# Optimization experiments

Hardware: AMD Instinct MI355X
Metric: run time of the kernel (lower is better)

Reference implementation:

```python
import jax, jax.numpy as jnp
import numpy as np

T = 4096; D = 768; V = 32000; L = 4; EPS = 1e-5


def _ln(x, g, b):
    m = jnp.mean(x, axis=-1, keepdims=True)
    v = jnp.mean((x - m) ** 2, axis=-1, keepdims=True)
    return (x - m) * jax.lax.rsqrt(v + EPS) * g + b


def _qgelu(x):
    return x * jax.nn.sigmoid(1.702 * x)


def setup_inputs() -> dict:
    key = jax.random.key(0)
    ks = jax.random.split(key, 10)
    s = 0.02
    return {
        "idx": jax.random.randint(ks[0], (T,), 0, V),
        "wte": jax.random.normal(ks[1], (V, D)) * s,
        "rb_ln_g": jnp.ones((D,)), "rb_ln_b": jnp.zeros((D,)),
        "rb_fc_w": jax.random.normal(ks[2], (D, 4 * D)) * s,
        "rb_fc_b": jnp.zeros((4 * D,)),
        "rb_proj_w": jax.random.normal(ks[3], (4 * D, D)) * s,
        "rb_proj_b": jnp.zeros((D,)),
        "lnf_g": jnp.ones((D,)), "lnf_b": jnp.zeros((D,)),
        "lm_head_w": jax.random.normal(ks[4], (D, V)) * s,
        "mb_ln_g": jnp.ones((L, 2 * D)), "mb_ln_b": jnp.zeros((L, 2 * D)),
        "mb_fc_w": jax.random.normal(ks[5], (L, 2 * D, 4 * D)) * s,
        "mb_fc_b": jnp.zeros((L, 4 * D)),
        "mb_proj_w": jax.random.normal(ks[6], (L, 4 * D, D)) * s,
        "mb_proj_b": jnp.zeros((L, D)),
        "op_w": jax.random.normal(ks[7], (L, D, D)) * s,
        "op_b": jnp.zeros((L, D)),
        "lns_g": jnp.ones((L, D)), "lns_b": jnp.zeros((L, D)),
        "heads_w": jax.random.normal(ks[8], (L, D, V)) * s,
    }


def reference(idx, wte, rb_ln_g, rb_ln_b, rb_fc_w, rb_fc_b, rb_proj_w, rb_proj_b,
              lnf_g, lnf_b, lm_head_w, mb_ln_g, mb_ln_b, mb_fc_w, mb_fc_b,
              mb_proj_w, mb_proj_b, op_w, op_b, lns_g, lns_b, heads_w):
    # token embedding (dropout is identity in eval) + initial residual block
    x = wte[idx]  # [T, D]
    h = _ln(x, rb_ln_g, rb_ln_b)
    x = x + _qgelu(h @ rb_fc_w + rb_fc_b) @ rb_proj_w + rb_proj_b
    x = _ln(x, lnf_g, lnf_b)
    logits = x @ lm_head_w  # [T, V]

    # targets=None path: pred_targets = cat(idx[1:], [-1])
    pred_targets = jnp.concatenate([idx[1:], jnp.full((1,), -1, idx.dtype)])
    pos = jnp.arange(T)
    skey = jax.random.key(42)

    for i in range(L):  # static small loop over layers
        j = i + 1
        # multinomial(softmax(logits), 1) == categorical(logits)
        idx_next = jax.random.categorical(jax.random.fold_in(skey, i), logits)
        # positions p where the sample matched the next-token target and p < T - j
        mask = (idx_next == pred_targets) & (pos < T - j)  # [T] bool
        # x2[p] = x[p + j] (padded); compute merge densely, select with mask
        x2 = jnp.concatenate([x[j:], jnp.zeros((j, D), x.dtype)], axis=0)
        h = _ln(jnp.concatenate([x, x2], axis=-1), mb_ln_g[i], mb_ln_b[i])
        merged = x2 + _qgelu(h @ mb_fc_w[i] + mb_fc_b[i]) @ mb_proj_w[i] + mb_proj_b[i]
        # scatter merged[p] into x at position p + j where mask[p]
        merged_s = jnp.concatenate([jnp.zeros((j, D), x.dtype), merged[:-j]], axis=0)
        mask_s = jnp.concatenate([jnp.zeros((j,), bool), mask[:-j]], axis=0)
        x = jnp.where(mask_s[:, None], merged_s, x)
        x = x @ op_w[i] + op_b[i]
        x = _ln(x, lns_g[i], lns_b[i])
        logits = x @ heads_w[i]
    return logits
```

## Files before the change

kernel.cpp:

```cpp
#include <hip/hip_runtime.h>
#include <cstdint>
#include <cstddef>

#define T_TOK 4096
#define DIM   768
#define VOCAB 32000
#define NLAYER 4
#define HALF_TV 65536000u

typedef short bf16x8 __attribute__((ext_vector_type(8)));
typedef float f32x4  __attribute__((ext_vector_type(4)));

__host__ __device__ inline void tf2x32(uint32_t k0, uint32_t k1, uint32_t& v0, uint32_t& v1){
  uint32_t ks2 = k0 ^ k1 ^ 0x1BD11BDAu;
  uint32_t x0 = v0 + k0, x1 = v1 + k1;
#define TFR(R) { x0 += x1; x1 = (x1<<R)|(x1>>(32-R)); x1 ^= x0; }
  TFR(13) TFR(15) TFR(26) TFR(6)
  x0 += k1;  x1 += ks2 + 1u;
  TFR(17) TFR(29) TFR(16) TFR(24)
  x0 += ks2; x1 += k0 + 2u;
  TFR(13) TFR(15) TFR(26) TFR(6)
  x0 += k0;  x1 += k1 + 3u;
  TFR(17) TFR(29) TFR(16) TFR(24)
  x0 += k1;  x1 += ks2 + 4u;
  TFR(13) TFR(15) TFR(26) TFR(6)
  x0 += ks2; x1 += k0 + 5u;
#undef TFR
  v0 = x0; v1 = x1;
}

__device__ inline void gumbel_pair(uint32_t kf0, uint32_t kf1, uint32_t t_up, uint32_t v,
                                   float& gu, float& gd){
  uint32_t m = t_up * (uint32_t)VOCAB + v;
  uint32_t x0 = m, x1 = m + HALF_TV;
  tf2x32(kf0, kf1, x0, x1);
  uint32_t ku = x0 >> 9, kd = x1 >> 9;
  float uu = ku ? (float)ku * 1.1920928955078125e-7f : 1.17549435082228751e-38f;
  float ud = kd ? (float)kd * 1.1920928955078125e-7f : 1.17549435082228751e-38f;
  gu = -logf(-logf(uu));
  gd = -logf(-logf(ud));
}

__device__ inline unsigned short f2bf(float f){
  uint32_t u = __float_as_uint(f);
  return (unsigned short)((u + 0x7FFFu + ((u >> 16) & 1u)) >> 16);
}
__device__ inline float bf2f(unsigned short h){
  return __uint_as_float(((uint32_t)h) << 16);
}
__device__ inline void cvt8(const float* f, bool lo, unsigned short* out){
  #pragma unroll
  for (int e=0;e<8;e++){
    float x = f[e];
    unsigned short h = f2bf(x);
    if (lo) h = f2bf(x - bf2f(h));
    out[e] = h;
  }
}
__device__ inline float blockReduceSum(float v){
  __shared__ float red[4];
  #pragma unroll
  for (int off=32; off>0; off>>=1) v += __shfl_down(v, off);
  int w = threadIdx.x >> 6;
  __syncthreads();
  if ((threadIdx.x & 63) == 0) red[w] = v;
  __syncthreads();
  return red[0] + red[1] + red[2] + red[3];
}

__device__ inline void gload16(const void* g, void* l){
  __builtin_amdgcn_global_load_lds(
      (const __attribute__((address_space(1))) unsigned int*)g,
      (__attribute__((address_space(3))) unsigned int*)l, 16, 0, 0);
}

enum { ST_F32 = 0, ST_HILO = 1, ST_SAMPLE = 2 };

template<int KSTEPS, int NSEG, bool BIAS, bool QGELU, bool RES, int STORE>
__global__ __launch_bounds__(256) void k_hgemm(
    const unsigned short* __restrict__ A0, const unsigned short* __restrict__ A1,
    const unsigned short* __restrict__ B0, const unsigned short* __restrict__ B2,
    float* __restrict__ C, unsigned short* __restrict__ Ch, unsigned short* __restrict__ Cl,
    const float* __restrict__ bias, const float* __restrict__ res,
    int N, uint32_t kf0, uint32_t kf1, unsigned long long* __restrict__ row_best)
{
  constexpr int K = KSTEPS * 64;
  __shared__ unsigned short sA[128*64];
  __shared__ unsigned short sB[128*64];
  const int t = threadIdx.x;
  const int wave = t >> 6, lane = t & 63;
  const int wm = wave >> 1, wn = wave & 1;
  const int g = lane >> 4, r = lane & 15;
  const int lr = lane >> 3, lc = lane & 7;

  int bid = blockIdx.x;
  int xcd = bid & 7, c = bid >> 3;
  int bm = xcd*4 + (c & 3);
  int bn = c >> 2;

  f32x4 acc[4][4] = {};

  for (int kb = 0; kb < NSEG*KSTEPS; ++kb){
    const int seg = (NSEG == 1) ? 0 : (kb / KSTEPS);
    const int k0  = (NSEG == 1) ? kb*64 : (kb % KSTEPS) * 64;
    const unsigned short* Ap = (seg == 1) ? A1 : A0;
    const unsigned short* Bp = (seg == 2) ? B2 : B0;
    __syncthreads();
    #pragma unroll
    for (int p=0;p<4;p++){
      int mr = p*32 + wave*8 + lr;
      int blk = mr >> 4;
      int grow = bm*64 + ((blk>>1)<<4) + (mr & 15) + ((blk & 1) ? 2048 : 0);
      int gk = k0 + ((lc ^ lr) << 3);
      gload16(Ap + (size_t)grow * K + gk, (char*)sA + mr*128 + lc*16);
      int nrow = bn*128 + mr;
      gload16(Bp + (size_t)nrow * K + gk, (char*)sB + mr*128 + lc*16);
    }
    __syncthreads();
    #pragma unroll
    for (int kk=0;kk<2;kk++){
      bf16x8 av[4], bv[4];
      #pragma unroll
      for (int mi=0;mi<4;mi++){
        int tr = wm*64 + mi*16 + r;
        av[mi] = *(const bf16x8*)((const char*)sA + tr*128 + (((kk*4+g) ^ (r&7))<<4));
      }
      #pragma unroll
      for (int ni=0;ni<4;ni++){
        int tr = wn*64 + ni*16 + r;
        bv[ni] = *(const bf16x8*)((const char*)sB + tr*128 + (((kk*4+g) ^ (r&7))<<4));
      }
      #pragma unroll
      for (int mi=0;mi<4;mi++)
        #pragma unroll
        for (int ni=0;ni<4;ni++)
          acc[mi][ni] = __builtin_amdgcn_mfma_f32_16x16x32_bf16(av[mi], bv[ni], acc[mi][ni], 0, 0, 0);
    }
  }

  if constexpr (STORE == ST_SAMPLE){
    #pragma unroll
    for (int mi=0; mi<4; mi+=2){
      int row16 = ((wm*4 + mi) >> 1) << 4;
      #pragma unroll
      for (int jj=0;jj<4;jj++){
        uint32_t t_up = bm*64 + row16 + g*4 + jj;
        unsigned long long bu = 0ull, bd = 0ull;
        #pragma unroll
        for (int ni=0;ni<4;ni++){
          uint32_t v = bn*128 + wn*64 + ni*16 + r;
          float gu, gd;
          gumbel_pair(kf0, kf1, t_up, v, gu, gd);
          float vu = acc[mi][ni][jj]   + gu;
          float vd = acc[mi+1][ni][jj] + gd;
          uint32_t fu = __float_as_uint(vu); fu = (fu & 0x80000000u) ? ~fu : (fu | 0x80000000u);
          uint32_t fd = __float_as_uint(vd); fd = (fd & 0x80000000u) ? ~fd : (fd | 0x80000000u);
          unsigned long long pu = ((unsigned long long)fu << 32) | (unsigned long long)(~v);
          unsigned long long pd = ((unsigned long long)fd << 32) | (unsigned long long)(~v);
          if (pu > bu) bu = pu;
          if (pd > bd) bd = pd;
        }
        #pragma unroll
        for (int off=1; off<16; off<<=1){
          unsigned int l0 = (unsigned int)bu, h0 = (unsigned int)(bu>>32);
          unsigned int l1 = __shfl_xor(l0, off), h1 = __shfl_xor(h0, off);
          unsigned long long o = ((unsigned long long)h1 << 32) | (unsigned long long)l1;
          if (o > bu) bu = o;
          l0 = (unsigned int)bd; h0 = (unsigned int)(bd>>32);
          l1 = __shfl_xor(l0, off); h1 = __shfl_xor(h0, off);
          o = ((unsigned long long)h1 << 32) | (unsigned long long)l1;
          if (o > bd) bd = o;
        }
        if (r == 0){
          atomicMax(&row_best[t_up], bu);
          atomicMax(&row_best[t_up + 2048], bd);
        }
      }
    }
  } else {
    #pragma unroll
    for (int mi=0;mi<4;mi++){
      int blk2 = wm*4 + mi;
      int mbase = bm*64 + ((blk2>>1)<<4) + ((blk2 & 1) ? 2048 : 0);
      #pragma unroll
      for (int ni=0;ni<4;ni++){
        int n = bn*128 + wn*64 + ni*16 + r;
        float bv_ = BIAS ? bias[n] : 0.0f;
        #pragma unroll
        for (int jj=0;jj<4;jj++){
          int m = mbase + g*4 + jj;
          float v = acc[mi][ni][jj] + bv_;
          if constexpr (QGELU) v = v / (1.0f + expf(-1.702f * v));
          if constexpr (RES)   v += res[(size_t)m * N + n];
          if constexpr (STORE == ST_F32){
            C[(size_t)m * N + n] = v;
          } else {
            unsigned short h = f2bf(v);
            Ch[(size_t)m * N + n] = h;
            Cl[(size_t)m * N + n] = f2bf(v - bf2f(h));
          }
        }
      }
    }
  }
}

template<bool SPLIT>
__global__ __launch_bounds__(256) void k_wt_t(const float* __restrict__ W,
    unsigned short* __restrict__ Bh, unsigned short* __restrict__ Bl, int K, int N)
{
  __shared__ unsigned short sH[64][72];
  __shared__ unsigned short sL[64][72];
  int kt = blockIdx.x, nt = blockIdx.y;
  int t = threadIdx.x;
  int kr = t >> 4, nc4 = (t & 15) * 4;
  #pragma unroll
  for (int p=0;p<4;p++){
    int k = p*16 + kr;
    float4 w = *(const float4*)&W[(size_t)(kt*64 + k) * N + nt*64 + nc4];
    const float* wf = (const float*)&w;
    #pragma unroll
    for (int e=0;e<4;e++){
      unsigned short h = f2bf(wf[e]);
      sH[nc4+e][k] = h;
      if (SPLIT) sL[nc4+e][k] = f2bf(wf[e] - bf2f(h));
    }
  }
  __syncthreads();
  #pragma unroll
  for (int q=0;q<2;q++){
    int cid = t + q*256;
    int n = cid >> 3, ch = cid & 7;
    *(bf16x8*)&Bh[(size_t)(nt*64+n)*K + kt*64 + ch*8] = *(const bf16x8*)&sH[n][ch*8];
    if (SPLIT)
      *(bf16x8*)&Bl[(size_t)(nt*64+n)*K + kt*64 + ch*8] = *(const bf16x8*)&sL[n][ch*8];
  }
}

__global__ __launch_bounds__(256) void k_embed_ln(const int* __restrict__ idx,
    const float* __restrict__ wte, const float* __restrict__ g, const float* __restrict__ b,
    float* __restrict__ Xraw, unsigned short* __restrict__ Hh, unsigned short* __restrict__ Hl)
{
  int row = blockIdx.x;
  const float* src = wte + (size_t)idx[row] * DIM;
  float v[3];
  #pragma unroll
  for (int jj=0;jj<3;jj++) v[jj] = src[threadIdx.x + jj*256];
  float s = blockReduceSum(v[0]+v[1]+v[2]);
  float mean = s * (1.0f/DIM);
  float s2 = 0;
  #pragma unroll
  for (int jj=0;jj<3;jj++){ float d = v[jj]-mean; s2 += d*d; }
  s2 = blockReduceSum(s2);
  float rs = rsqrtf(s2 * (1.0f/DIM) + 1e-5f);
  #pragma unroll
  for (int jj=0;jj<3;jj++){
    int d = threadIdx.x + jj*256;
    Xraw[(size_t)row*DIM + d] = v[jj];
    float o = (v[jj]-mean)*rs*g[d] + b[d];
    unsigned short h = f2bf(o);
    Hh[(size_t)row*DIM + d] = h;
    Hl[(size_t)row*DIM + d] = f2bf(o - bf2f(h));
  }
}

__global__ __launch_bounds__(256) void k_ln(const float* __restrict__ in, float* __restrict__ out,
    const float* __restrict__ g, const float* __restrict__ b,
    unsigned short* __restrict__ obf, unsigned short* __restrict__ olo)
{
  int row = blockIdx.x;
  const float* src = in + (size_t)row * DIM;
  float v[3];
  #pragma unroll
  for (int jj=0;jj<3;jj++) v[jj] = src[threadIdx.x + jj*256];
  float s = blockReduceSum(v[0]+v[1]+v[2]);
  float mean = s * (1.0f/DIM);
  float s2 = 0;
  #pragma unroll
  for (int jj=0;jj<3;jj++){ float d = v[jj]-mean; s2 += d*d; }
  s2 = blockReduceSum(s2);
  float rs = rsqrtf(s2 * (1.0f/DIM) + 1e-5f);
  #pragma unroll
  for (int jj=0;jj<3;jj++){
    int d = threadIdx.x + jj*256;
    float o = (v[jj]-mean)*rs*g[d] + b[d];
    out[(size_t)row*DIM + d] = o;
    unsigned short h = f2bf(o);
    obf[(size_t)row*DIM + d] = h;
    olo[(size_t)row*DIM + d] = f2bf(o - bf2f(h));
  }
}

__global__ void k_mask(const unsigned long long* __restrict__ row_best,
    const int* __restrict__ idx, int j, int* __restrict__ count, int* __restrict__ plist)
{
  int t = blockIdx.x * blockDim.x + threadIdx.x;
  if (t >= T_TOK) return;
  int v = (int)(~(uint32_t)(row_best[t] & 0xFFFFFFFFull));
  int tgt = (t < T_TOK-1) ? idx[t+1] : -1;
  if (v == tgt && t < T_TOK - j){
    int pos = atomicAdd(count, 1);
    plist[pos] = t;
  }
}

__global__ __launch_bounds__(256) void k_merge(const float* __restrict__ X,
    const int* __restrict__ plist, const int* __restrict__ count,
    const float* __restrict__ lng, const float* __restrict__ lnb,
    const float* __restrict__ fcw, const float* __restrict__ fcb,
    const float* __restrict__ pjw, const float* __restrict__ pjb,
    float* __restrict__ mergebuf, int j)
{
  __shared__ float sh[1536 + 3072];
  int nb = *count;
  for (int bIdx = blockIdx.x; bIdx < nb; bIdx += gridDim.x){
    int p = plist[bIdx];
    const float* xp = X + (size_t)p * DIM;
    const float* x2 = X + (size_t)(p + j) * DIM;
    for (int d = threadIdx.x; d < 1536; d += 256)
      sh[d] = (d < DIM) ? xp[d] : x2[d - DIM];
    __syncthreads();
    float s = 0;
    for (int d = threadIdx.x; d < 1536; d += 256) s += sh[d];
    s = blockReduceSum(s);
    float mean = s * (1.0f/1536.0f);
    float s2 = 0;
    for (int d = threadIdx.x; d < 1536; d += 256){ float df = sh[d]-mean; s2 += df*df; }
    s2 = blockReduceSum(s2);
    float rs = rsqrtf(s2 * (1.0f/1536.0f) + 1e-5f);
    __syncthreads();
    for (int d = threadIdx.x; d < 1536; d += 256)
      sh[d] = (sh[d]-mean)*rs*lng[d] + lnb[d];
    __syncthreads();
    float* act = sh + 1536;
    #pragma unroll
    for (int jj=0;jj<12;jj++){
      int n = threadIdx.x + jj*256;
      float a = fcb[n];
      for (int k=0;k<1536;k++) a += sh[k]*fcw[(size_t)k*3072 + n];
      act[n] = a / (1.0f + expf(-1.702f*a));
    }
    __syncthreads();
    #pragma unroll
    for (int jj=0;jj<3;jj++){
      int d = threadIdx.x + jj*256;
      float a = pjb[d];
      for (int k=0;k<3072;k++) a += act[k]*pjw[(size_t)k*DIM + d];
      mergebuf[(size_t)bIdx*DIM + d] = x2[d] + a;
    }
    __syncthreads();
  }
}

__global__ void k_scatter(float* __restrict__ X, unsigned short* __restrict__ Xbf,
    unsigned short* __restrict__ Xlo, const float* __restrict__ mergebuf,
    const int* __restrict__ plist, const int* __restrict__ count, int j)
{
  int nb = *count;
  for (int bIdx = blockIdx.x; bIdx < nb; bIdx += gridDim.x){
    int p = plist[bIdx];
    for (int d = threadIdx.x; d < DIM; d += 256){
      float v = mergebuf[(size_t)bIdx*DIM + d];
      size_t o = (size_t)(p + j)*DIM + d;
      X[o] = v;
      unsigned short h = f2bf(v);
      Xbf[o] = h;
      Xlo[o] = f2bf(v - bf2f(h));
    }
  }
}

__global__ __launch_bounds__(256) void k_gemm_old(
    const float* __restrict__ A, const float* __restrict__ B, float* __restrict__ C,
    int M, int N, int K)
{
  __shared__ unsigned short sA[128*64];
  __shared__ unsigned short sB[128*64];
  const int t = threadIdx.x;
  const int bn = blockIdx.x, bm = blockIdx.y;
  const int wave = t >> 6, lane = t & 63;
  const int wm = wave >> 1, wn = wave & 1;
  const int g = lane >> 4, r = lane & 15;
  f32x4 acc[4][4] = {};
  const int nK = K >> 6;
  const int aC = t & 7,  aM0 = t >> 3;
  const int bN0 = t & 31, bC = t >> 5;
  const float* Abase = A + (size_t)(bm*128) * K;
  const float* Bbase = B + (size_t)(bn*128);
  for (int seg = 0; seg < 3; ++seg) {
    const bool aLO = (seg == 1), bLO = (seg == 2);
    for (int kb = 0; kb < nK; ++kb) {
      const int k0 = kb << 6;
      __syncthreads();
      #pragma unroll
      for (int p=0;p<4;p++){
        int m = p*32 + aM0;
        const float* src = Abase + (size_t)m * K + k0 + aC*8;
        float ff[8];
        *(float4*)(ff)   = *(const float4*)(src);
        *(float4*)(ff+4) = *(const float4*)(src+4);
        unsigned short hh[8];
        cvt8(ff, aLO, hh);
        *(bf16x8*)&sA[m*64 + ((aC ^ (m & 7)) * 8)] = *(bf16x8*)hh;
      }
      #pragma unroll
      for (int p=0;p<4;p++){
        int n = p*32 + bN0;
        float ff[8];
        const float* src = Bbase + (size_t)(k0 + bC*8) * N + n;
        #pragma unroll
        for (int e=0;e<8;e++) ff[e] = src[(size_t)e * N];
        unsigned short hh[8];
        cvt8(ff, bLO, hh);
        *(bf16x8*)&sB[n*64 + ((bC ^ (n & 7)) * 8)] = *(bf16x8*)hh;
      }
      __syncthreads();
      #pragma unroll
      for (int kk=0;kk<2;kk++){
        bf16x8 av[4], bv[4];
        #pragma unroll
        for (int mi=0;mi<4;mi++){
          int m = wm*64 + mi*16 + r;
          av[mi] = *(const bf16x8*)&sA[m*64 + (((kk*4 + g) ^ (m & 7)) * 8)];
        }
        #pragma unroll
        for (int ni=0;ni<4;ni++){
          int n = wn*64 + ni*16 + r;
          bv[ni] = *(const bf16x8*)&sB[n*64 + (((kk*4 + g) ^ (n & 7)) * 8)];
        }
        #pragma unroll
        for (int mi=0;mi<4;mi++)
          #pragma unroll
          for (int ni=0;ni<4;ni++)
            acc[mi][ni] = __builtin_amdgcn_mfma_f32_16x16x32_bf16(av[mi], bv[ni], acc[mi][ni], 0, 0, 0);
      }
    }
  }
  #pragma unroll
  for (int mi=0;mi<4;mi++)
    #pragma unroll
    for (int ni=0;ni<4;ni++)
      #pragma unroll
      for (int jj=0;jj<4;jj++){
        int m = bm*128 + wm*64 + mi*16 + g*4 + jj;
        int n = bn*128 + wn*64 + ni*16 + r;
        C[(size_t)m * N + n] = acc[mi][ni][jj];
      }
}

static void fold_key(uint32_t i, uint32_t& o0, uint32_t& o1){
  uint32_t x0 = 0, x1 = i;
  tf2x32(0u, 42u, x0, x1);
  o0 = x0; o1 = x1;
}

extern "C" void kernel_launch(void* const* d_in, const int* in_sizes, int n_in,
                              void* d_out, int out_size, void* d_ws, size_t ws_size,
                              hipStream_t stream)
{
  const int*   idx       = (const int*)  d_in[0];
  const float* wte       = (const float*)d_in[1];
  const float* rb_ln_g   = (const float*)d_in[2];
  const float* rb_ln_b   = (const float*)d_in[3];
  const float* rb_fc_w   = (const float*)d_in[4];
  const float* rb_fc_b   = (const float*)d_in[5];
  const float* rb_proj_w = (const float*)d_in[6];
  const float* rb_proj_b = (const float*)d_in[7];
  const float* lnf_g     = (const float*)d_in[8];
  const float* lnf_b     = (const float*)d_in[9];
  const float* lm_head_w = (const float*)d_in[10];
  const float* mb_ln_g   = (const float*)d_in[11];
  const float* mb_ln_b   = (const float*)d_in[12];
  const float* mb_fc_w   = (const float*)d_in[13];
  const float* mb_fc_b   = (const float*)d_in[14];
  const float* mb_proj_w = (const float*)d_in[15];
  const float* mb_proj_b = (const float*)d_in[16];
  const float* op_w      = (const float*)d_in[17];
  const float* op_b      = (const float*)d_in[18];
  const float* lns_g     = (const float*)d_in[19];
  const float* lns_b     = (const float*)d_in[20];
  const float* heads_w   = (const float*)d_in[21];

  const size_t TD = (size_t)T_TOK * DIM;
  const size_t DV = (size_t)DIM * VOCAB;

  float* X = (float*)d_ws;
  float* Y = X + TD;
  unsigned short* Xbf = (unsigned short*)(Y + TD);
  unsigned short* Xlo = Xbf + TD;
  unsigned short* BtFh = Xlo + TD;
  unsigned short* BtFl = BtFh + DV;
  size_t need_big = (size_t)((char*)(BtFl + DV) - (char*)d_ws);
  bool big = ws_size >= need_big;

  char* ob = (char*)d_out;
  float* OUT = (float*)d_out;
  unsigned short* Hh     = (unsigned short*)(ob);
  unsigned short* Hl     = Hh + TD;
  unsigned short* ACTh   = (unsigned short*)(ob + ((size_t)16<<20));
  unsigned short* ACTl   = ACTh + TD*4;
  unsigned short* Btfc_h = (unsigned short*)(ob + ((size_t)72<<20));
  unsigned short* Btfc_l = Btfc_h + (size_t)3072*DIM;
  unsigned short* Btpj_h = (unsigned short*)(ob + ((size_t)84<<20));
  unsigned short* Btpj_l = Btpj_h + (size_t)3072*DIM;
  unsigned short* BtS    = (unsigned short*)(ob + ((size_t)96<<20));
  unsigned short* Btop_h = (unsigned short*)(ob + ((size_t)152<<20));
  unsigned short* Btop_l = Btop_h + (size_t)DIM*DIM;
  float* MERGE = (float*)(ob + ((size_t)160<<20));
  unsigned long long* ROWBEST = (unsigned long long*)(ob + ((size_t)176<<20));
  int* PLIST = (int*)(ROWBEST + T_TOK);
  int* COUNT = PLIST + T_TOK;

  dim3 blk(256);

  k_embed_ln<<<T_TOK, blk, 0, stream>>>(idx, wte, rb_ln_g, rb_ln_b, X, Hh, Hl);
  k_wt_t<true><<<dim3(12,48), blk, 0, stream>>>(rb_fc_w,   Btfc_h, Btfc_l, DIM,  3072);
  k_wt_t<true><<<dim3(48,12), blk, 0, stream>>>(rb_proj_w, Btpj_h, Btpj_l, 3072, DIM);
  k_hgemm<12,3,true,true,false,ST_HILO><<<24*32, blk, 0, stream>>>(
      Hh, Hl, Btfc_h, Btfc_l, nullptr, ACTh, ACTl, rb_fc_b, nullptr, 3072, 0u,0u, nullptr);
  k_hgemm<48,3,true,false,true,ST_F32><<<6*32, blk, 0, stream>>>(
      ACTh, ACTl, Btpj_h, Btpj_l, Y, nullptr, nullptr, rb_proj_b, X, DIM, 0u,0u, nullptr);
  k_ln<<<T_TOK, blk, 0, stream>>>(Y, X, lnf_g, lnf_b, Xbf, Xlo);

  for (int i = 0; i < NLAYER; ++i){
    int j = i + 1;
    uint32_t kf0, kf1; fold_key((uint32_t)i, kf0, kf1);

    hipMemsetAsync(ROWBEST, 0, (size_t)T_TOK*8, stream);
    hipMemsetAsync(COUNT, 0, 4, stream);

    const float* hw = (i == 0) ? lm_head_w : heads_w + (size_t)(i-1)*DV;
    k_wt_t<false><<<dim3(12,500), blk, 0, stream>>>(hw, BtS, nullptr, DIM, VOCAB);
    k_hgemm<12,1,false,false,false,ST_SAMPLE><<<250*32, blk, 0, stream>>>(
        Xbf, Xbf, BtS, BtS, nullptr, nullptr, nullptr, nullptr, nullptr,
        VOCAB, kf0, kf1, ROWBEST);

    k_mask<<<T_TOK/256, blk, 0, stream>>>(ROWBEST, idx, j, COUNT, PLIST);
    k_merge<<<64, blk, 0, stream>>>(X, PLIST, COUNT,
        mb_ln_g + (size_t)i*1536, mb_ln_b + (size_t)i*1536,
        mb_fc_w + (size_t)i*1536*3072, mb_fc_b + (size_t)i*3072,
        mb_proj_w + (size_t)i*3072*DIM, mb_proj_b + (size_t)i*DIM, MERGE, j);
    k_scatter<<<64, blk, 0, stream>>>(X, Xbf, Xlo, MERGE, PLIST, COUNT, j);

    k_wt_t<true><<<dim3(12,12), blk, 0, stream>>>(op_w + (size_t)i*DIM*DIM, Btop_h, Btop_l, DIM, DIM);
    k_hgemm<12,3,true,false,false,ST_F32><<<6*32, blk, 0, stream>>>(
        Xbf, Xlo, Btop_h, Btop_l, Y, nullptr, nullptr, op_b + (size_t)i*DIM, nullptr,
        DIM, 0u,0u, nullptr);
    k_ln<<<T_TOK, blk, 0, stream>>>(Y, X, lns_g + (size_t)i*DIM, lns_b + (size_t)i*DIM, Xbf, Xlo);
  }

  if (big){
    k_wt_t<true><<<dim3(12,500), blk, 0, stream>>>(heads_w + (size_t)3*DV, BtFh, BtFl, DIM, VOCAB);
    k_hgemm<12,3,false,false,false,ST_F32><<<250*32, blk, 0, stream>>>(
        Xbf, Xlo, BtFh, BtFl, OUT, nullptr, nullptr, nullptr, nullptr, VOCAB, 0u,0u, nullptr);
  } else {
    k_gemm_old<<<dim3(VOCAB/128, T_TOK/128), blk, 0, stream>>>(
        X, heads_w + (size_t)3*DV, OUT, T_TOK, VOCAB, DIM);
  }
}
```

Before: 3.072 ms.

## Cheaper Gumbel log math, MFMA priority, and nontemporal loads/stores

Replaces the double logf in Gumbel noise generation with hardware log2 plus a series expansion near u=1, avoiding the full-precision libm log. Raises wave priority around the MFMA block in the sampling GEMM so matrix work can overlap the heavy epilogue of other waves. Adds nontemporal stores for the final logits output and nontemporal loads in the weight transpose to reduce cache pollution. The approximate log could change sampled tokens near ties compared with the reference.

```diff
diff --git a/kernel.cpp b/kernel.cpp
--- a/kernel.cpp
+++ b/kernel.cpp
@@ -10,6 +10,7 @@
 
 typedef short bf16x8 __attribute__((ext_vector_type(8)));
 typedef float f32x4  __attribute__((ext_vector_type(4)));
+typedef float f32x4v __attribute__((ext_vector_type(4)));
 
 __host__ __device__ inline void tf2x32(uint32_t k0, uint32_t k1, uint32_t& v0, uint32_t& v1){
   uint32_t ks2 = k0 ^ k1 ^ 0x1BD11BDAu;
@@ -29,16 +30,28 @@
   v0 = x0; v1 = x1;
 }
 
+__device__ inline float neglog_u(uint32_t k){
+  float L;
+  if (k >= 0x780000u){
+    float x = (float)(0x800000u - k) * 1.1920928955078125e-7f;
+    L = x * fmaf(x, fmaf(x, fmaf(x, 0.25f, 0.3333333333333f), 0.5f), 1.0f);
+  } else {
+    float l2k = __builtin_amdgcn_logf((float)k);
+    L = 0.69314718055994531f * (23.0f - l2k);
+    if (k == 0u) L = 87.33654475055310898f;
+  }
+  return L;
+}
+
 __device__ inline void gumbel_pair(uint32_t kf0, uint32_t kf1, uint32_t t_up, uint32_t v,
                                    float& gu, float& gd){
   uint32_t m = t_up * (uint32_t)VOCAB + v;
   uint32_t x0 = m, x1 = m + HALF_TV;
   tf2x32(kf0, kf1, x0, x1);
-  uint32_t ku = x0 >> 9, kd = x1 >> 9;
-  float uu = ku ? (float)ku * 1.1920928955078125e-7f : 1.17549435082228751e-38f;
-  float ud = kd ? (float)kd * 1.1920928955078125e-7f : 1.17549435082228751e-38f;
-  gu = -logf(-logf(uu));
-  gd = -logf(-logf(ud));
+  float Lu = neglog_u(x0 >> 9);
+  float Ld = neglog_u(x1 >> 9);
+  gu = -0.69314718055994531f * __builtin_amdgcn_logf(Lu);
+  gd = -0.69314718055994531f * __builtin_amdgcn_logf(Ld);
 }
 
 __device__ inline unsigned short f2bf(float f){
@@ -76,7 +89,7 @@
 
 enum { ST_F32 = 0, ST_HILO = 1, ST_SAMPLE = 2 };
 
-template<int KSTEPS, int NSEG, bool BIAS, bool QGELU, bool RES, int STORE>
+template<int KSTEPS, int NSEG, bool BIAS, bool QGELU, bool RES, int STORE, bool NTST>
 __global__ __launch_bounds__(256) void k_hgemm(
     const unsigned short* __restrict__ A0, const unsigned short* __restrict__ A1,
     const unsigned short* __restrict__ B0, const unsigned short* __restrict__ B2,
@@ -130,11 +143,13 @@
         int tr = wn*64 + ni*16 + r;
         bv[ni] = *(const bf16x8*)((const char*)sB + tr*128 + (((kk*4+g) ^ (r&7))<<4));
       }
+      if constexpr (STORE == ST_SAMPLE) __builtin_amdgcn_s_setprio(1);
       #pragma unroll
       for (int mi=0;mi<4;mi++)
         #pragma unroll
         for (int ni=0;ni<4;ni++)
           acc[mi][ni] = __builtin_amdgcn_mfma_f32_16x16x32_bf16(av[mi], bv[ni], acc[mi][ni], 0, 0, 0);
+      if constexpr (STORE == ST_SAMPLE) __builtin_amdgcn_s_setprio(0);
     }
   }
 
@@ -193,7 +208,8 @@
           if constexpr (QGELU) v = v / (1.0f + expf(-1.702f * v));
           if constexpr (RES)   v += res[(size_t)m * N + n];
           if constexpr (STORE == ST_F32){
-            C[(size_t)m * N + n] = v;
+            if constexpr (NTST) __builtin_nontemporal_store(v, &C[(size_t)m * N + n]);
+            else                C[(size_t)m * N + n] = v;
           } else {
             unsigned short h = f2bf(v);
             Ch[(size_t)m * N + n] = h;
@@ -217,13 +233,12 @@
   #pragma unroll
   for (int p=0;p<4;p++){
     int k = p*16 + kr;
-    float4 w = *(const float4*)&W[(size_t)(kt*64 + k) * N + nt*64 + nc4];
-    const float* wf = (const float*)&w;
+    f32x4v w = __builtin_nontemporal_load((const f32x4v*)&W[(size_t)(kt*64 + k) * N + nt*64 + nc4]);
     #pragma unroll
     for (int e=0;e<4;e++){
-      unsigned short h = f2bf(wf[e]);
+      unsigned short h = f2bf(w[e]);
       sH[nc4+e][k] = h;
-      if (SPLIT) sL[nc4+e][k] = f2bf(wf[e] - bf2f(h));
+      if (SPLIT) sL[nc4+e][k] = f2bf(w[e] - bf2f(h));
     }
   }
   __syncthreads();
@@ -516,9 +531,9 @@
   k_embed_ln<<<T_TOK, blk, 0, stream>>>(idx, wte, rb_ln_g, rb_ln_b, X, Hh, Hl);
   k_wt_t<true><<<dim3(12,48), blk, 0, stream>>>(rb_fc_w,   Btfc_h, Btfc_l, DIM,  3072);
   k_wt_t<true><<<dim3(48,12), blk, 0, stream>>>(rb_proj_w, Btpj_h, Btpj_l, 3072, DIM);
-  k_hgemm<12,3,true,true,false,ST_HILO><<<24*32, blk, 0, stream>>>(
+  k_hgemm<12,3,true,true,false,ST_HILO,false><<<24*32, blk, 0, stream>>>(
       Hh, Hl, Btfc_h, Btfc_l, nullptr, ACTh, ACTl, rb_fc_b, nullptr, 3072, 0u,0u, nullptr);
-  k_hgemm<48,3,true,false,true,ST_F32><<<6*32, blk, 0, stream>>>(
+  k_hgemm<48,3,true,false,true,ST_F32,false><<<6*32, blk, 0, stream>>>(
       ACTh, ACTl, Btpj_h, Btpj_l, Y, nullptr, nullptr, rb_proj_b, X, DIM, 0u,0u, nullptr);
   k_ln<<<T_TOK, blk, 0, stream>>>(Y, X, lnf_g, lnf_b, Xbf, Xlo);
 
@@ -531,7 +546,7 @@
 
     const float* hw = (i == 0) ? lm_head_w : heads_w + (size_t)(i-1)*DV;
     k_wt_t<false><<<dim3(12,500), blk, 0, stream>>>(hw, BtS, nullptr, DIM, VOCAB);
-    k_hgemm<12,1,false,false,false,ST_SAMPLE><<<250*32, blk, 0, stream>>>(
+    k_hgemm<12,1,false,false,false,ST_SAMPLE,false><<<250*32, blk, 0, stream>>>(
         Xbf, Xbf, BtS, BtS, nullptr, nullptr, nullptr, nullptr, nullptr,
         VOCAB, kf0, kf1, ROWBEST);
 
@@ -543,7 +558,7 @@
     k_scatter<<<64, blk, 0, stream>>>(X, Xbf, Xlo, MERGE, PLIST, COUNT, j);
 
     k_wt_t<true><<<dim3(12,12), blk, 0, stream>>>(op_w + (size_t)i*DIM*DIM, Btop_h, Btop_l, DIM, DIM);
-    k_hgemm<12,3,true,false,false,ST_F32><<<6*32, blk, 0, stream>>>(
+    k_hgemm<12,3,true,false,false,ST_F32,false><<<6*32, blk, 0, stream>>>(
         Xbf, Xlo, Btop_h, Btop_l, Y, nullptr, nullptr, op_b + (size_t)i*DIM, nullptr,
         DIM, 0u,0u, nullptr);
     k_ln<<<T_TOK, blk, 0, stream>>>(Y, X, lns_g + (size_t)i*DIM, lns_b + (size_t)i*DIM, Xbf, Xlo);
@@ -551,7 +566,7 @@
 
   if (big){
     k_wt_t<true><<<dim3(12,500), blk, 0, stream>>>(heads_w + (size_t)3*DV, BtFh, BtFl, DIM, VOCAB);
-    k_hgemm<12,3,false,false,false,ST_F32><<<250*32, blk, 0, stream>>>(
+    k_hgemm<12,3,false,false,false,ST_F32,true><<<250*32, blk, 0, stream>>>(
         Xbf, Xlo, BtFh, BtFl, OUT, nullptr, nullptr, nullptr, nullptr, VOCAB, 0u,0u, nullptr);
   } else {
     k_gemm_old<<<dim3(VOCAB/128, T_TOK/128), blk, 0, stream>>>(
```

New measurement: 2.817 ms. 8.3% less time.
